# Kernel tuning notes

Hardware: AMD Instinct MI355X
Metric: run time of the kernel (lower is better)

## Reference

```python
import math
import jax, jax.numpy as jnp
import numpy as np

B, N, C = 2, 2048, 768
H, DH = 12, 64  # num_heads, head_dim


def setup_inputs() -> dict:
    key = jax.random.key(0)
    ks = jax.random.split(key, 5)
    s = 1.0 / math.sqrt(C)  # keep linear outputs O(1)
    return {
        "x": jax.random.normal(ks[0], (B, N, C), jnp.float32),
        "Wq": jax.random.normal(ks[1], (C, C), jnp.float32) * s,
        "bq": jnp.zeros((C,), jnp.float32),
        "Wk": jax.random.normal(ks[2], (C, C), jnp.float32) * s,
        "bk": jnp.zeros((C,), jnp.float32),
        "Wv": jax.random.normal(ks[3], (C, C), jnp.float32) * s,
        "bv": jnp.zeros((C,), jnp.float32),
        "Wp": jax.random.normal(ks[4], (C, C), jnp.float32) * s,
        "bp": jnp.zeros((C,), jnp.float32),
    }


def reference(x, Wq, bq, Wk, bk, Wv, bv, Wp, bp):
    # Linear projections; torch nn.Linear computes x @ W.T + b, here W stored
    # as (in, out) so it's x @ W + b with equivalent math.
    def split(t):  # [B,N,C] -> [B,H,N,DH]
        return t.reshape(B, N, H, DH).transpose(0, 2, 1, 3)

    q = split(x @ Wq + bq)
    k = split(x @ Wk + bk)
    v = split(x @ Wv + bv)
    scale = 1.0 / math.sqrt(DH)
    attn = jnp.einsum("bhqd,bhkd->bhqk", q, k) * scale  # [B,H,N,N]
    attn = jax.nn.softmax(attn, axis=-1)  # attn_drop=0.0 -> identity
    y = jnp.einsum("bhqk,bhkd->bhqd", attn, v)  # [B,H,N,DH]
    y = y.transpose(0, 2, 1, 3).reshape(B, N, C)
    return y @ Wp + bp  # proj_drop=0.0 -> identity
```

## Files before the change

kernel.cpp:

```cpp
#include <hip/hip_runtime.h>


typedef __bf16 bf16_t;
typedef __bf16 bf16x8 __attribute__((ext_vector_type(8)));
typedef __bf16 bf16x4 __attribute__((ext_vector_type(4)));
typedef short  short4_t __attribute__((ext_vector_type(4)));
typedef float  floatx4 __attribute__((ext_vector_type(4)));

#define MFMA32(a, b, c) __builtin_amdgcn_mfma_f32_16x16x32_bf16(a, b, c, 0, 0, 0)
#define MFMA16(a, b, c) __builtin_amdgcn_mfma_f32_16x16x16bf16_1k(a, b, c, 0, 0, 0)

__device__ __forceinline__ void gload16(const bf16_t* g, bf16_t* l) {
  __builtin_amdgcn_global_load_lds(
      (__attribute__((address_space(1))) void*)g,
      (__attribute__((address_space(3))) void*)l, 16, 0, 0);
}

__global__ __launch_bounds__(256) void cvt_x_kernel(const float* __restrict__ x,
                                                    bf16_t* __restrict__ xb) {
  int i = blockIdx.x * 256 + threadIdx.x;
  floatx4 v = ((const floatx4*)x)[i];
  bf16x4 o;
  o[0] = (bf16_t)v[0]; o[1] = (bf16_t)v[1]; o[2] = (bf16_t)v[2]; o[3] = (bf16_t)v[3];
  ((bf16x4*)xb)[i] = o;
}

__global__ __launch_bounds__(256) void cvt_wt_kernel(
    const float* __restrict__ W0, const float* __restrict__ W1,
    const float* __restrict__ W2, const float* __restrict__ W3,
    bf16_t* __restrict__ T0, bf16_t* __restrict__ T1,
    bf16_t* __restrict__ T2, bf16_t* __restrict__ T3) {
  const int z = blockIdx.z;
  const float* W = (z == 0) ? W0 : (z == 1) ? W1 : (z == 2) ? W2 : W3;
  bf16_t* WT = (z == 0) ? T0 : (z == 1) ? T1 : (z == 2) ? T2 : T3;
  __shared__ bf16_t T[64][65];
  const int c = threadIdx.x & 63, r0 = threadIdx.x >> 6;
  const int i0 = blockIdx.y * 64, o0 = blockIdx.x * 64;
#pragma unroll
  for (int p = 0; p < 16; ++p) {
    int r = p * 4 + r0;
    T[r][c] = (bf16_t)W[(i0 + r) * 768 + o0 + c];
  }
  __syncthreads();
#pragma unroll
  for (int p = 0; p < 16; ++p) {
    int r = p * 4 + r0;
    WT[(o0 + r) * 768 + i0 + c] = T[c][r];
  }
}


__global__ __launch_bounds__(256) void gemm_qkv(
    const bf16_t* __restrict__ Xb, const bf16_t* __restrict__ WqT,
    const bf16_t* __restrict__ WkT, const bf16_t* __restrict__ WvT,
    const float* __restrict__ bq, const float* __restrict__ bk,
    const float* __restrict__ bv, bf16_t* __restrict__ qw,
    bf16_t* __restrict__ kw, bf16_t* __restrict__ vtw) {
  __shared__ bf16_t Al[128 * 64];
  __shared__ bf16_t Bl[128 * 64];
  const int z = blockIdx.z;
  const bf16_t* Wt = (z == 0) ? WqT : (z == 1) ? WkT : WvT;
  const float* bias = (z == 0) ? bq : (z == 1) ? bk : bv;
  const float oscale = (z == 0) ? 0.18033688011112042f : 1.0f;

  const int tid = threadIdx.x, lane = tid & 63, w = tid >> 6;
  const int wr = w >> 1, wc = w & 1;
  const int l15 = lane & 15, quad = lane >> 4;
  const int m0 = blockIdx.y * 128, n0 = blockIdx.x * 128;

  const bf16_t* ga = &Wt[(m0 + w * 32 + (lane >> 3)) * 768 + (lane & 7) * 8];
  const bf16_t* gb = &Xb[(n0 + w * 32 + (lane >> 3)) * 768 + (lane & 7) * 8];
  bf16_t* la = &Al[w * 32 * 64];
  bf16_t* lb = &Bl[w * 32 * 64];

  floatx4 acc[4][4] = {};

  for (int kt = 0; kt < 768; kt += 64) {
#pragma unroll
    for (int p = 0; p < 4; ++p) {
      gload16(ga + p * 8 * 768 + kt, la + p * 8 * 64);
      gload16(gb + p * 8 * 768 + kt, lb + p * 8 * 64);
    }
    __syncthreads();
#pragma unroll
    for (int kk = 0; kk < 2; ++kk) {
      bf16x8 af[4], bfr[4];
#pragma unroll
      for (int i = 0; i < 4; ++i) {
        af[i]  = *(bf16x8*)&Al[(wr * 64 + i * 16 + l15) * 64 + kk * 32 + quad * 8];
        bfr[i] = *(bf16x8*)&Bl[(wc * 64 + i * 16 + l15) * 64 + kk * 32 + quad * 8];
      }
#pragma unroll
      for (int mi = 0; mi < 4; ++mi)
#pragma unroll
        for (int ni = 0; ni < 4; ++ni)
          acc[mi][ni] = MFMA32(af[mi], bfr[ni], acc[mi][ni]);
    }
    __syncthreads();
  }

  const int hh = (m0 + wr * 64) >> 6;
#pragma unroll
  for (int mi = 0; mi < 4; ++mi) {
    const int d0 = mi * 16 + quad * 4;
    const int gm0 = m0 + wr * 64 + d0;
    float bv4[4];
#pragma unroll
    for (int r = 0; r < 4; ++r) bv4[r] = bias[gm0 + r];
#pragma unroll
    for (int ni = 0; ni < 4; ++ni) {
      const int gn = n0 + wc * 64 + ni * 16 + l15;
      const int bb = gn >> 11, tok = gn & 2047;
      const int bh = bb * 12 + hh;
      if (z == 0) {
        bf16x4 pk;
#pragma unroll
        for (int r = 0; r < 4; ++r)
          pk[r] = (bf16_t)((acc[mi][ni][r] + bv4[r]) * oscale);
        *(bf16x4*)&qw[bh * 131072 + tok * 64 + d0] = pk;
      } else if (z == 1) {
        const int kt2 = tok >> 7, k128 = tok & 127;
        const int nk = k128 >> 4, kl15 = k128 & 15;
        const int kk = d0 >> 5, kq = (d0 >> 3) & 3, j0 = d0 & 7;
        bf16x4 pk;
#pragma unroll
        for (int r = 0; r < 4; ++r)
          pk[r] = (bf16_t)(acc[mi][ni][r] + bv4[r]);
        *(bf16x4*)&kw[bh * 131072 + kt2 * 8192 +
                      ((nk * 2 + kk) * 64 + kq * 16 + kl15) * 8 + j0] = pk;
      } else {
        const int kt2 = tok >> 7, k128 = tok & 127;
        const int nk = k128 >> 4, vq = (k128 >> 2) & 3, j = k128 & 3;
        const int nd = d0 >> 4, vl0 = d0 & 15;
        const int base = bh * 131072 + kt2 * 8192 +
                         ((nk * 4 + nd) * 64 + vq * 16 + vl0) * 4 + j;
#pragma unroll
        for (int r = 0; r < 4; ++r)
          vtw[base + r * 4] = (bf16_t)(acc[mi][ni][r] + bv4[r]);
      }
    }
  }
}

__global__ __launch_bounds__(256) void gemm_proj(
    const bf16_t* __restrict__ Yb, const bf16_t* __restrict__ WpT,
    const float* __restrict__ bias, float* __restrict__ out) {
  __shared__ bf16_t Al[128 * 64];
  __shared__ bf16_t Bl[128 * 64];
  const int tid = threadIdx.x, lane = tid & 63, w = tid >> 6;
  const int wr = w >> 1, wc = w & 1;
  const int l15 = lane & 15, quad = lane >> 4;
  const int m0 = blockIdx.y * 128, n0 = blockIdx.x * 128;

  const bf16_t* ga = &WpT[(m0 + w * 32 + (lane >> 3)) * 768 + (lane & 7) * 8];
  const bf16_t* gb = &Yb[(n0 + w * 32 + (lane >> 3)) * 768 + (lane & 7) * 8];
  bf16_t* la = &Al[w * 32 * 64];
  bf16_t* lb = &Bl[w * 32 * 64];

  floatx4 acc[4][4] = {};

  for (int kt = 0; kt < 768; kt += 64) {
#pragma unroll
    for (int p = 0; p < 4; ++p) {
      gload16(ga + p * 8 * 768 + kt, la + p * 8 * 64);
      gload16(gb + p * 8 * 768 + kt, lb + p * 8 * 64);
    }
    __syncthreads();
#pragma unroll
    for (int kk = 0; kk < 2; ++kk) {
      bf16x8 af[4], bfr[4];
#pragma unroll
      for (int i = 0; i < 4; ++i) {
        af[i]  = *(bf16x8*)&Al[(wr * 64 + i * 16 + l15) * 64 + kk * 32 + quad * 8];
        bfr[i] = *(bf16x8*)&Bl[(wc * 64 + i * 16 + l15) * 64 + kk * 32 + quad * 8];
      }
#pragma unroll
      for (int mi = 0; mi < 4; ++mi)
#pragma unroll
        for (int ni = 0; ni < 4; ++ni)
          acc[mi][ni] = MFMA32(af[mi], bfr[ni], acc[mi][ni]);
    }
    __syncthreads();
  }

#pragma unroll
  for (int mi = 0; mi < 4; ++mi) {
    const int gm0 = m0 + wr * 64 + mi * 16 + quad * 4;
    floatx4 bv4;
#pragma unroll
    for (int r = 0; r < 4; ++r) bv4[r] = bias[gm0 + r];
#pragma unroll
    for (int ni = 0; ni < 4; ++ni) {
      const int gn = n0 + wc * 64 + ni * 16 + l15;
      floatx4 v = acc[mi][ni] + bv4;
      *(floatx4*)&out[gn * 768 + gm0] = v;
    }
  }
}

__global__ __launch_bounds__(256, 3) void attn_kernel(
    const bf16_t* __restrict__ Q, const bf16_t* __restrict__ Kf,
    const bf16_t* __restrict__ Vf, bf16_t* __restrict__ Y) {
  __shared__ __align__(16) float Ox[4096];
  __shared__ float Ls[2][2][2][16];

  const int tid = threadIdx.x, lane = tid & 63, w = tid >> 6;
  const int wq = w & 1, wk = w >> 1;
  const int l15 = lane & 15, quad = lane >> 4;
  const int bh = blockIdx.y;
  const int q0 = blockIdx.x * 64;
  const bf16_t* Qb = Q + bh * 131072;
  const bf16_t* Kb = Kf + bh * 131072 + wk * 4096 + lane * 8;
  const bf16_t* Vb = Vf + bh * 131072 + wk * 4096 + lane * 4;

  bf16x8 qf[2][2];
#pragma unroll
  for (int ni = 0; ni < 2; ++ni)
#pragma unroll
    for (int kk = 0; kk < 2; ++kk)
      qf[ni][kk] = *(const bf16x8*)&Qb[(q0 + wq * 32 + ni * 16 + l15) * 64 +
                                       kk * 32 + quad * 8];

  floatx4 oacc[2][4] = {};
  float lsum[2] = {0.f, 0.f};

  for (int kt = 0; kt < 16; ++kt) {
    const bf16_t* kg = Kb + kt * 8192;
    const bf16_t* vg = Vb + kt * 8192;

    bf16x8 kfr[4][2];
#pragma unroll
    for (int mt = 0; mt < 4; ++mt)
#pragma unroll
      for (int kk = 0; kk < 2; ++kk)
        kfr[mt][kk] = *(const bf16x8*)&kg[(mt * 2 + kk) * 512];
    bf16x4 vfr[4][4];
#pragma unroll
    for (int mt = 0; mt < 4; ++mt)
#pragma unroll
      for (int nd = 0; nd < 4; ++nd)
        vfr[mt][nd] = *(const bf16x4*)&vg[(mt * 4 + nd) * 256];

    short4_t pk[4][2];
#pragma unroll
    for (int mt = 0; mt < 4; ++mt) {
      floatx4 s[2] = {};
      __builtin_amdgcn_s_setprio(1);
#pragma unroll
      for (int kk = 0; kk < 2; ++kk)
#pragma unroll
        for (int ni = 0; ni < 2; ++ni)
          s[ni] = MFMA32(kfr[mt][kk], qf[ni][kk], s[ni]);
      __builtin_amdgcn_s_setprio(0);
#pragma unroll
      for (int ni = 0; ni < 2; ++ni) {
        bf16x4 ph;
#pragma unroll
        for (int r = 0; r < 4; ++r) {
          const float pv = __builtin_amdgcn_exp2f(s[ni][r]);
          lsum[ni] += pv;
          ph[r] = (bf16_t)pv;
        }
        pk[mt][ni] = __builtin_bit_cast(short4_t, ph);
      }
    }

    __builtin_amdgcn_s_setprio(1);
#pragma unroll
    for (int mt = 0; mt < 4; ++mt)
#pragma unroll
      for (int nd = 0; nd < 4; ++nd) {
        short4_t vs = __builtin_bit_cast(short4_t, vfr[mt][nd]);
#pragma unroll
        for (int ni = 0; ni < 2; ++ni)
          oacc[ni][nd] = MFMA16(pk[mt][ni], vs, oacc[ni][nd]);
      }
    __builtin_amdgcn_s_setprio(0);
  }

#pragma unroll
  for (int ni = 0; ni < 2; ++ni) {
    lsum[ni] += __shfl_xor(lsum[ni], 16);
    lsum[ni] += __shfl_xor(lsum[ni], 32);
  }
  if (quad == 0) {
#pragma unroll
    for (int ni = 0; ni < 2; ++ni) Ls[wq][wk][ni][l15] = lsum[ni];
  }

#pragma unroll
  for (int ni = 0; ni < 2; ++ni)
#pragma unroll
    for (int ndl = 0; ndl < 2; ++ndl) {
      const int nd = (1 - wk) * 2 + ndl;
      *(floatx4*)&Ox[((((wq * 2 + wk) * 2 + ni) * 2 + ndl) * 64 + lane) * 4] =
          oacc[ni][nd];
    }
  __syncthreads();

  const int bb = bh / 12, h = bh % 12;
#pragma unroll
  for (int ni = 0; ni < 2; ++ni) {
    float tot[4];
#pragma unroll
    for (int r = 0; r < 4; ++r)
      tot[r] = Ls[wq][0][ni][quad * 4 + r] + Ls[wq][1][ni][quad * 4 + r];
#pragma unroll
    for (int ndl = 0; ndl < 2; ++ndl) {
      const int nd = wk * 2 + ndl;
      floatx4 o = oacc[ni][nd];
      floatx4 other =
          *(floatx4*)&Ox[((((wq * 2 + (1 - wk)) * 2 + ni) * 2 + ndl) * 64 + lane) * 4];
      o += other;
#pragma unroll
      for (int r = 0; r < 4; ++r) {
        const int tok = q0 + wq * 32 + ni * 16 + quad * 4 + r;
        const int col = h * 64 + nd * 16 + l15;
        Y[(bb * 2048 + tok) * 768 + col] = (bf16_t)(o[r] / tot[r]);
      }
    }
  }
}

extern "C" void kernel_launch(void* const* d_in, const int* in_sizes, int n_in,
                              void* d_out, int out_size, void* d_ws, size_t ws_size,
                              hipStream_t stream) {
  const float* x  = (const float*)d_in[0];
  const float* Wq = (const float*)d_in[1];
  const float* bq = (const float*)d_in[2];
  const float* Wk = (const float*)d_in[3];
  const float* bk = (const float*)d_in[4];
  const float* Wv = (const float*)d_in[5];
  const float* bv = (const float*)d_in[6];
  const float* Wp = (const float*)d_in[7];
  const float* bp = (const float*)d_in[8];
  float* out = (float*)d_out;

  char* ws = (char*)d_ws;
  bf16_t* xb  = (bf16_t*)ws; ws += (size_t)4096 * 768 * 2;
  bf16_t* WqT = (bf16_t*)ws; ws += (size_t)768 * 768 * 2;
  bf16_t* WkT = (bf16_t*)ws; ws += (size_t)768 * 768 * 2;
  bf16_t* WvT = (bf16_t*)ws; ws += (size_t)768 * 768 * 2;
  bf16_t* WpT = (bf16_t*)ws; ws += (size_t)768 * 768 * 2;
  bf16_t* qw  = (bf16_t*)ws; ws += (size_t)24 * 2048 * 64 * 2;
  bf16_t* kw  = (bf16_t*)ws; ws += (size_t)24 * 2048 * 64 * 2;
  bf16_t* vtw = (bf16_t*)ws; ws += (size_t)24 * 2048 * 64 * 2;
  bf16_t* yw  = (bf16_t*)ws; ws += (size_t)4096 * 768 * 2;

  cvt_x_kernel<<<3072, 256, 0, stream>>>(x, xb);
  cvt_wt_kernel<<<dim3(12, 12, 4), 256, 0, stream>>>(Wq, Wk, Wv, Wp, WqT, WkT, WvT, WpT);

  gemm_qkv<<<dim3(32, 6, 3), 256, 0, stream>>>(xb, WqT, WkT, WvT, bq, bk, bv, qw, kw, vtw);
  attn_kernel<<<dim3(32, 24), 256, 0, stream>>>(qw, kw, vtw, yw);
  gemm_proj<<<dim3(32, 6), 256, 0, stream>>>(yw, WpT, bp, out);
}
```

Before: 193.9 us.

## Double-buffer K/V register loads, compute row sums via MFMA, remap blocks per XCD

The attention kernel now loads the next K/V tile into a second register set while computing the current one, so global load latency overlaps with MFMA work. The softmax row sums come from an extra MFMA against a ones vector instead of scalar adds followed by shuffles. The grid is flattened and each block index is remapped so that all query blocks of a head land on the same XCD, which should improve L2 reuse of K/V. The cost is roughly doubled K/V register use, which may hurt occupancy at the launch bound of 3 blocks per CU, plus a few extra MFMAs per tile.

New measurement: 248.5 us. 28.2% more time.

```diff
diff --git a/kernel.cpp b/kernel.cpp
--- a/kernel.cpp
+++ b/kernel.cpp
@@ -207,8 +207,12 @@
   const int tid = threadIdx.x, lane = tid & 63, w = tid >> 6;
   const int wq = w & 1, wk = w >> 1;
   const int l15 = lane & 15, quad = lane >> 4;
-  const int bh = blockIdx.y;
-  const int q0 = blockIdx.x * 64;
+
+  const int i = blockIdx.x;
+  const int xcd = i & 7, j = i >> 3;
+  const int bh = xcd * 3 + (j >> 5);
+  const int q0 = (j & 31) * 64;
+
   const bf16_t* Qb = Q + bh * 131072;
   const bf16_t* Kb = Kf + bh * 131072 + wk * 4096 + lane * 8;
   const bf16_t* Vb = Vf + bh * 131072 + wk * 4096 + lane * 4;
@@ -222,25 +226,24 @@
                                        kk * 32 + quad * 8];
 
   floatx4 oacc[2][4] = {};
-  float lsum[2] = {0.f, 0.f};
-
-  for (int kt = 0; kt < 16; ++kt) {
+  floatx4 sacc[2] = {};
+  const short4_t ones = {0x3F80, 0x3F80, 0x3F80, 0x3F80};
+
+  auto loadkv = [&](bf16x8 (&kf)[4][2], bf16x4 (&vf)[4][4], int kt) {
     const bf16_t* kg = Kb + kt * 8192;
     const bf16_t* vg = Vb + kt * 8192;
-
-    bf16x8 kfr[4][2];
-#pragma unroll
-    for (int mt = 0; mt < 4; ++mt)
+#pragma unroll
+    for (int mt = 0; mt < 4; ++mt) {
 #pragma unroll
       for (int kk = 0; kk < 2; ++kk)
-        kfr[mt][kk] = *(const bf16x8*)&kg[(mt * 2 + kk) * 512];
-    bf16x4 vfr[4][4];
-#pragma unroll
-    for (int mt = 0; mt < 4; ++mt)
+        kf[mt][kk] = *(const bf16x8*)&kg[(mt * 2 + kk) * 512];
 #pragma unroll
       for (int nd = 0; nd < 4; ++nd)
-        vfr[mt][nd] = *(const bf16x4*)&vg[(mt * 4 + nd) * 256];
-
+        vf[mt][nd] = *(const bf16x4*)&vg[(mt * 4 + nd) * 256];
+    }
+  };
+
+  auto compute = [&](const bf16x8 (&kf)[4][2], const bf16x4 (&vf)[4][4]) {
     short4_t pk[4][2];
 #pragma unroll
     for (int mt = 0; mt < 4; ++mt) {
@@ -250,42 +253,52 @@
       for (int kk = 0; kk < 2; ++kk)
 #pragma unroll
         for (int ni = 0; ni < 2; ++ni)
-          s[ni] = MFMA32(kfr[mt][kk], qf[ni][kk], s[ni]);
+          s[ni] = MFMA32(kf[mt][kk], qf[ni][kk], s[ni]);
       __builtin_amdgcn_s_setprio(0);
 #pragma unroll
       for (int ni = 0; ni < 2; ++ni) {
         bf16x4 ph;
 #pragma unroll
-        for (int r = 0; r < 4; ++r) {
-          const float pv = __builtin_amdgcn_exp2f(s[ni][r]);
-          lsum[ni] += pv;
-          ph[r] = (bf16_t)pv;
-        }
+        for (int r = 0; r < 4; ++r)
+          ph[r] = (bf16_t)__builtin_amdgcn_exp2f(s[ni][r]);
         pk[mt][ni] = __builtin_bit_cast(short4_t, ph);
       }
     }
 
     __builtin_amdgcn_s_setprio(1);
 #pragma unroll
-    for (int mt = 0; mt < 4; ++mt)
+    for (int mt = 0; mt < 4; ++mt) {
 #pragma unroll
       for (int nd = 0; nd < 4; ++nd) {
-        short4_t vs = __builtin_bit_cast(short4_t, vfr[mt][nd]);
+        short4_t vs = __builtin_bit_cast(short4_t, vf[mt][nd]);
 #pragma unroll
         for (int ni = 0; ni < 2; ++ni)
           oacc[ni][nd] = MFMA16(pk[mt][ni], vs, oacc[ni][nd]);
       }
+#pragma unroll
+      for (int ni = 0; ni < 2; ++ni)
+        sacc[ni] = MFMA16(pk[mt][ni], ones, sacc[ni]);
+    }
     __builtin_amdgcn_s_setprio(0);
-  }
-
-#pragma unroll
-  for (int ni = 0; ni < 2; ++ni) {
-    lsum[ni] += __shfl_xor(lsum[ni], 16);
-    lsum[ni] += __shfl_xor(lsum[ni], 32);
-  }
-  if (quad == 0) {
-#pragma unroll
-    for (int ni = 0; ni < 2; ++ni) Ls[wq][wk][ni][l15] = lsum[ni];
+  };
+
+  bf16x8 kA[4][2], kB[4][2];
+  bf16x4 vA[4][4], vB[4][4];
+  loadkv(kA, vA, 0);
+#pragma unroll
+  for (int kt = 0; kt < 16; kt += 2) {
+    loadkv(kB, vB, kt + 1);
+    compute(kA, vA);
+    if (kt + 2 < 16) loadkv(kA, vA, kt + 2);
+    compute(kB, vB);
+  }
+
+  if (l15 == 0) {
+#pragma unroll
+    for (int ni = 0; ni < 2; ++ni)
+#pragma unroll
+      for (int r = 0; r < 4; ++r)
+        Ls[wq][wk][ni][quad * 4 + r] = sacc[ni][r];
   }
 
 #pragma unroll
@@ -351,6 +364,6 @@
   cvt_wt_kernel<<<dim3(12, 12, 4), 256, 0, stream>>>(Wq, Wk, Wv, Wp, WqT, WkT, WvT, WpT);
 
   gemm_qkv<<<dim3(32, 6, 3), 256, 0, stream>>>(xb, WqT, WkT, WvT, bq, bk, bv, qw, kw, vtw);
-  attn_kernel<<<dim3(32, 24), 256, 0, stream>>>(qw, kw, vtw, yw);
+  attn_kernel<<<768, 256, 0, stream>>>(qw, kw, vtw, yw);
   gemm_proj<<<dim3(32, 6), 256, 0, stream>>>(yw, WpT, bp, out);
 }
```
